# Kernel tuning notes

Hardware: AMD Instinct MI355X
Metric: run time of the kernel (lower is better)

## Reference

```python
import jax, jax.numpy as jnp
import numpy as np

EPS_COS = 1e-8   # torch F.cosine_similarity norm clamp
EPS_LN = 1e-5    # torch LayerNorm eps


def setup_inputs() -> dict:
    key = jax.random.key(0)
    ks = jax.random.split(key, 8)
    B, P, T, D, H = 512, 200000, 4, 64, 256
    return {
        "target_feat": jax.random.normal(ks[0], (B, D), jnp.float32),
        "source_protos": jax.random.normal(ks[1], (P, T, D), jnp.float32),
        "W1": jax.random.normal(ks[2], (3 * D, H), jnp.float32) * 0.05,
        "b1": jnp.zeros((H,), jnp.float32),
        "ln_g": jnp.ones((H,), jnp.float32),
        "ln_b": jnp.zeros((H,), jnp.float32),
        "W2": jax.random.normal(ks[3], (H, H), jnp.float32) * 0.05,
        "b2": jnp.zeros((H,), jnp.float32),
        "W3": jax.random.normal(ks[4], (H, D), jnp.float32) * 0.05,
        "b3": jnp.zeros((D,), jnp.float32),
        "top_k": 3,
    }


def _layernorm(x, g, b):
    mu = jnp.mean(x, axis=-1, keepdims=True)
    var = jnp.mean(jnp.square(x - mu), axis=-1, keepdims=True)
    return (x - mu) * jax.lax.rsqrt(var + EPS_LN) * g + b


def reference(target_feat, source_protos, W1, b1, ln_g, ln_b, W2, b2, W3, b3, top_k):
    # --- retrieve_similar_prototypes (batched over B queries) ---
    centers = jnp.mean(source_protos, axis=1)              # [P, D]
    tn = target_feat / jnp.maximum(
        jnp.linalg.norm(target_feat, axis=-1, keepdims=True), EPS_COS)
    cn = centers / jnp.maximum(
        jnp.linalg.norm(centers, axis=-1, keepdims=True), EPS_COS)
    sims = jnp.einsum("bd,pd->bp", tn, cn)                 # [B, P] cosine sims
    top_vals, top_idx = jax.lax.top_k(sims, top_k)         # [B, K]
    similar_protos = centers[top_idx]                      # [B, K, D] gather

    # --- interpolate_new_prototype ---
    weights = jax.nn.softmax(top_vals, axis=-1)            # [B, K]
    weighted = jnp.einsum("bkd,bk->bd", similar_protos, weights)
    concat = jnp.concatenate(
        [weighted, similar_protos[:, 0], target_feat], axis=-1)  # [B, 3D]

    h = jax.nn.relu(_layernorm(concat @ W1 + b1, ln_g, ln_b))
    h = jax.nn.relu(h @ W2 + b2)
    new_proto = h @ W3 + b3                                # [B, D]
    return new_proto
```

## Files before the change

kernel.cpp:

```cpp
#include <hip/hip_runtime.h>

#define PTOT 200000
#define NB 512
#define DD 64
#define PT 256
#define NBLK ((PTOT + PT - 1) / PT)
#define NCAND 8

typedef __attribute__((ext_vector_type(4))) float f32x4;
typedef __attribute__((ext_vector_type(8))) __bf16 bf16x8;

__device__ __forceinline__ ushort f2bf(float f){
  uint u = __float_as_uint(f);
  u += 0x7FFFu + ((u >> 16) & 1u);
  return (ushort)(u >> 16);
}

__device__ __forceinline__ uint mkkey(float v, int plocal){
  uint u = __float_as_uint(v);
  u = (u & 0xFFFFFE00u) | (uint)plocal;
  return u ^ (uint)(((int)u >> 31) | 0x80000000);
}

__device__ __forceinline__ void ins3(uint& k0, uint& k1, uint& k2, uint key){
  uint t0 = k0 > key ? k0 : key;
  uint m0 = k0 > key ? key : k0;
  uint t1 = k1 > m0 ? k1 : m0;
  uint m1 = k1 > m0 ? m0 : k1;
  k2 = k2 > m1 ? k2 : m1;
  k1 = t1; k0 = t0;
}

__global__ __launch_bounds__(64) void k0_tn(const float* __restrict__ tf,
                                            float* __restrict__ tnf,
                                            ushort* __restrict__ tnb){
  int b = blockIdx.x, d = threadIdx.x;
  float v = tf[b * DD + d];
  float ss = v * v;
  #pragma unroll
  for (int m = 1; m < 64; m <<= 1) ss += __shfl_xor(ss, m, 64);
  float rn = 1.0f / fmaxf(sqrtf(ss), 1e-8f);
  float t = v * rn;
  tnf[b * DD + d] = t;
  tnb[b * DD + d] = f2bf(t);
}

__global__ __launch_bounds__(256) void k1_scan(const float* __restrict__ sp,
                                               const ushort* __restrict__ tnb,
                                               uint* __restrict__ cand){
  __shared__ ushort cn[PT * 64];
  __shared__ uint kbuf[4][NB][3];
  const int tid = threadIdx.x;
  const int blk = blockIdx.x;
  const int pbase = blk * PT;
  const int plim = min(PT, PTOT - pbase);

  {
    const int s = tid & 15;
    const int pg = tid >> 4;
    for (int pass = 0; pass < 16; ++pass){
      int pl = pass * 16 + pg;
      f32x4 c = {0.f, 0.f, 0.f, 0.f};
      if (pl < plim){
        const float* base = sp + (size_t)(pbase + pl) * 256 + s * 4;
        f32x4 a0 = *(const f32x4*)(base);
        f32x4 a1 = *(const f32x4*)(base + 64);
        f32x4 a2 = *(const f32x4*)(base + 128);
        f32x4 a3 = *(const f32x4*)(base + 192);
        c = ((a0 + a1) + (a2 + a3)) * 0.25f;
      }
      float ss2 = c.x*c.x + c.y*c.y + c.z*c.z + c.w*c.w;
      ss2 += __shfl_xor(ss2, 1, 64);
      ss2 += __shfl_xor(ss2, 2, 64);
      ss2 += __shfl_xor(ss2, 4, 64);
      ss2 += __shfl_xor(ss2, 8, 64);
      float rn = 1.0f / fmaxf(sqrtf(ss2), 1e-8f);
      ushort4 h;
      h.x = f2bf(c.x * rn); h.y = f2bf(c.y * rn);
      h.z = f2bf(c.z * rn); h.w = f2bf(c.w * rn);
      int byteo = (pl * 128 + s * 8) ^ ((pl & 7) << 4);
      *(ushort4*)((char*)cn + byteo) = h;
    }
  }
  __syncthreads();

  const int wave = tid >> 6;
  const int lane = tid & 63;
  const int l15 = lane & 15;
  const int lg  = lane >> 4;
  const int wpb = wave * 64;

  bf16x8 afrag[4][2];
  #pragma unroll
  for (int ps = 0; ps < 4; ++ps){
    #pragma unroll
    for (int kh = 0; kh < 2; ++kh){
      int p = wpb + ps * 16 + l15;
      int byteo = (p * 128 + (kh * 32 + lg * 8) * 2) ^ ((p & 7) << 4);
      afrag[ps][kh] = *(const bf16x8*)((const char*)cn + byteo);
    }
  }

  const int lbase = lg * 4;
  for (int bt = 0; bt < 32; ++bt){
    const ushort* tp = tnb + (size_t)(bt * 16 + l15) * 64 + lg * 8;
    bf16x8 bf0 = *(const bf16x8*)(tp);
    bf16x8 bf1 = *(const bf16x8*)(tp + 32);
    f32x4 acc[4];
    #pragma unroll
    for (int ps = 0; ps < 4; ++ps){
      f32x4 z = {0.f, 0.f, 0.f, 0.f};
      acc[ps] = __builtin_amdgcn_mfma_f32_16x16x32_bf16(afrag[ps][0], bf0, z, 0, 0, 0);
      acc[ps] = __builtin_amdgcn_mfma_f32_16x16x32_bf16(afrag[ps][1], bf1, acc[ps], 0, 0, 0);
    }
    uint k0 = 0, k1 = 0, k2 = 0;
    #pragma unroll
    for (int ps = 0; ps < 4; ++ps){
      #pragma unroll
      for (int j = 0; j < 4; ++j){
        int plocal = wpb + ps * 16 + lbase + j;
        uint key = mkkey(acc[ps][j], plocal);
        key = (plocal < plim) ? key : 0u;
        ins3(k0, k1, k2, key);
      }
    }
    #pragma unroll
    for (int m = 16; m <= 32; m <<= 1){
      uint o0 = (uint)__shfl_xor((int)k0, m, 64);
      uint o1 = (uint)__shfl_xor((int)k1, m, 64);
      uint o2 = (uint)__shfl_xor((int)k2, m, 64);
      ins3(k0, k1, k2, o0);
      ins3(k0, k1, k2, o1);
      ins3(k0, k1, k2, o2);
    }
    if (lane < 16){
      int b = bt * 16 + l15;
      kbuf[wave][b][0] = k0;
      kbuf[wave][b][1] = k1;
      kbuf[wave][b][2] = k2;
    }
  }
  __syncthreads();
  for (int b = tid; b < NB; b += 256){
    uint k0 = 0, k1 = 0, k2 = 0;
    #pragma unroll
    for (int w = 0; w < 4; ++w){
      ins3(k0, k1, k2, kbuf[w][b][0]);
      ins3(k0, k1, k2, kbuf[w][b][1]);
      ins3(k0, k1, k2, kbuf[w][b][2]);
    }
    uint* dst = cand + ((size_t)b * NBLK + blk) * 3;
    dst[0] = k0; dst[1] = k1; dst[2] = k2;
  }
}

__global__ __launch_bounds__(256) void k2_rerank(const uint* __restrict__ cand,
    const float* __restrict__ sp, const float* __restrict__ tnf,
    const float* __restrict__ tf, float* __restrict__ concat){
  __shared__ uint pool[NBLK * 3];
  __shared__ uint redk[4];
  __shared__ int redp[4];
  __shared__ int topp[NCAND];
  __shared__ float cen[NCAND][DD];
  __shared__ float esim[NCAND];
  __shared__ float wts[3];
  __shared__ int sel[3];
  const int b = blockIdx.x;
  const int tid = threadIdx.x;
  const int NP = NBLK * 3;
  for (int j = tid; j < NP; j += 256) pool[j] = cand[(size_t)b * NP + j];
  __syncthreads();
  const int lane = tid & 63, wave = tid >> 6;
  for (int it = 0; it < NCAND; ++it){
    uint bk = 0; int bp = 0;
    for (int j = tid; j < NP; j += 256){
      uint k = pool[j];
      if (k > bk){ bk = k; bp = j; }
    }
    #pragma unroll
    for (int m = 1; m < 64; m <<= 1){
      uint ok = (uint)__shfl_xor((int)bk, m, 64);
      int  op = __shfl_xor(bp, m, 64);
      if (ok > bk){ bk = ok; bp = op; }
    }
    if (lane == 0){ redk[wave] = bk; redp[wave] = bp; }
    __syncthreads();
    if (tid == 0){
      uint bbk = 0; int bbp = 0;
      #pragma unroll
      for (int w = 0; w < 4; ++w){
        if (redk[w] > bbk){ bbk = redk[w]; bbp = redp[w]; }
      }
      topp[it] = (bbp / 3) * PT + (int)(bbk & 0x1FFu);
      pool[bbp] = 0u;
    }
    __syncthreads();
  }
  for (int c = wave; c < NCAND; c += 4){
    int p = topp[c];
    const float* base = sp + (size_t)p * 256 + lane;
    float x = 0.25f * (base[0] + base[64] + base[128] + base[192]);
    float ss = x * x;
    float dt = x * tnf[b * DD + lane];
    #pragma unroll
    for (int m = 1; m < 64; m <<= 1){
      ss += __shfl_xor(ss, m, 64);
      dt += __shfl_xor(dt, m, 64);
    }
    cen[c][lane] = x;
    if (lane == 0) esim[c] = dt / fmaxf(sqrtf(ss), 1e-8f);
  }
  __syncthreads();
  if (tid == 0){
    float v0 = -3.0e38f, v1 = v0, v2 = v0;
    int s0 = 0, s1 = 0, s2 = 0;
    for (int c = 0; c < NCAND; ++c){
      float v = esim[c];
      if (v > v0){ v2=v1; s2=s1; v1=v0; s1=s0; v0=v; s0=c; }
      else if (v > v1){ v2=v1; s2=s1; v1=v; s1=c; }
      else if (v > v2){ v2=v; s2=c; }
    }
    float e1 = expf(v1 - v0), e2 = expf(v2 - v0);
    float inv = 1.0f / (1.0f + e1 + e2);
    wts[0] = inv; wts[1] = e1 * inv; wts[2] = e2 * inv;
    sel[0] = s0; sel[1] = s1; sel[2] = s2;
  }
  __syncthreads();
  if (tid < DD){
    float w0 = wts[0], w1 = wts[1], w2 = wts[2];
    float c0 = cen[sel[0]][tid], c1 = cen[sel[1]][tid], c2 = cen[sel[2]][tid];
    float* row = concat + (size_t)b * 192;
    row[tid]       = w0 * c0 + w1 * c1 + w2 * c2;
    row[DD + tid]  = c0;
    row[128 + tid] = tf[b * DD + tid];
  }
}

__global__ __launch_bounds__(256) void k3_mlp(const float* __restrict__ concat,
    const float* __restrict__ W1, const float* __restrict__ b1,
    const float* __restrict__ lng, const float* __restrict__ lnb,
    const float* __restrict__ W2, const float* __restrict__ b2,
    const float* __restrict__ W3, const float* __restrict__ b3,
    float* __restrict__ out){
  __shared__ float cc[4][192];
  __shared__ float h1[4][256];
  __shared__ float h2[4][256];
  const int tid = threadIdx.x;
  const int rb = blockIdx.x * 4;
  for (int j = tid; j < 4 * 192; j += 256)
    cc[j / 192][j % 192] = concat[(size_t)rb * 192 + j];
  __syncthreads();
  {
    const int h = tid;
    float a0 = b1[h]; float a1 = a0, a2 = a0, a3 = a0;
    for (int k = 0; k < 192; ++k){
      float w = W1[k * 256 + h];
      a0 = fmaf(cc[0][k], w, a0);
      a1 = fmaf(cc[1][k], w, a1);
      a2 = fmaf(cc[2][k], w, a2);
      a3 = fmaf(cc[3][k], w, a3);
    }
    h1[0][h] = a0; h1[1][h] = a1; h1[2][h] = a2; h1[3][h] = a3;
  }
  __syncthreads();
  {
    const int lane = tid & 63, w = tid >> 6;
    float v[4]; float s = 0.f, q = 0.f;
    #pragma unroll
    for (int j = 0; j < 4; ++j){
      v[j] = h1[w][lane + 64 * j];
      s += v[j]; q += v[j] * v[j];
    }
    #pragma unroll
    for (int m = 1; m < 64; m <<= 1){
      s += __shfl_xor(s, m, 64);
      q += __shfl_xor(q, m, 64);
    }
    float mu = s * (1.0f / 256.0f);
    float var = q * (1.0f / 256.0f) - mu * mu;
    float rs = rsqrtf(var + 1e-5f);
    #pragma unroll
    for (int j = 0; j < 4; ++j){
      int hh = lane + 64 * j;
      float y = (v[j] - mu) * rs * lng[hh] + lnb[hh];
      h1[w][hh] = fmaxf(y, 0.0f);
    }
  }
  __syncthreads();
  {
    const int h = tid;
    float a0 = b2[h]; float a1 = a0, a2 = a0, a3 = a0;
    for (int k = 0; k < 256; ++k){
      float w = W2[k * 256 + h];
      a0 = fmaf(h1[0][k], w, a0);
      a1 = fmaf(h1[1][k], w, a1);
      a2 = fmaf(h1[2][k], w, a2);
      a3 = fmaf(h1[3][k], w, a3);
    }
    h2[0][h] = fmaxf(a0, 0.f); h2[1][h] = fmaxf(a1, 0.f);
    h2[2][h] = fmaxf(a2, 0.f); h2[3][h] = fmaxf(a3, 0.f);
  }
  __syncthreads();
  {
    const int d = tid & 63, q = tid >> 6;
    float a = b3[d];
    for (int k = 0; k < 256; ++k)
      a = fmaf(h2[q][k], W3[k * 64 + d], a);
    out[(size_t)(rb + q) * 64 + d] = a;
  }
}

extern "C" void kernel_launch(void* const* d_in, const int* in_sizes, int n_in,
                              void* d_out, int out_size, void* d_ws, size_t ws_size,
                              hipStream_t stream){
  const float* tf = (const float*)d_in[0];
  const float* sp = (const float*)d_in[1];
  const float* W1 = (const float*)d_in[2];
  const float* b1 = (const float*)d_in[3];
  const float* lng = (const float*)d_in[4];
  const float* lnb = (const float*)d_in[5];
  const float* W2 = (const float*)d_in[6];
  const float* b2 = (const float*)d_in[7];
  const float* W3 = (const float*)d_in[8];
  const float* b3 = (const float*)d_in[9];
  float* out = (float*)d_out;

  char* ws = (char*)d_ws;
  const size_t off_tnb = 0;
  const size_t off_tnf = 65536;
  const size_t off_cand = 65536 + 131072;
  const size_t off_cc = off_cand + (size_t)NB * NBLK * 3 * 4;
  const size_t need = off_cc + (size_t)NB * 192 * 4;
  if (ws_size < need) return;

  ushort* tnb = (ushort*)(ws + off_tnb);
  float* tnf = (float*)(ws + off_tnf);
  uint* cand = (uint*)(ws + off_cand);
  float* cc = (float*)(ws + off_cc);

  k0_tn<<<NB, 64, 0, stream>>>(tf, tnf, tnb);
  k1_scan<<<NBLK, 256, 0, stream>>>(sp, tnb, cand);
  k2_rerank<<<NB, 256, 0, stream>>>(cand, sp, tnf, tf, cc);
  k3_mlp<<<NB / 4, 256, 0, stream>>>(cc, W1, b1, lng, lnb, W2, b2, W3, b3, out);
}
```

Before: 135.1 us.

## Split center computation into separate kernel and restructure scan per-wave over queries

```diff
diff --git a/kernel.cpp b/kernel.cpp
--- a/kernel.cpp
+++ b/kernel.cpp
@@ -45,6 +45,109 @@
   tnb[b * DD + d] = f2bf(t);
 }
 
+__global__ __launch_bounds__(256) void k1a_centers(const float* __restrict__ sp,
+                                                   ushort* __restrict__ cn){
+  int gid = blockIdx.x * 256 + threadIdx.x;
+  int p = gid >> 4, s = gid & 15;
+  f32x4 c = {0.f, 0.f, 0.f, 0.f};
+  if (p < PTOT){
+    const float* base = sp + (size_t)p * 256 + s * 4;
+    f32x4 a0 = *(const f32x4*)(base);
+    f32x4 a1 = *(const f32x4*)(base + 64);
+    f32x4 a2 = *(const f32x4*)(base + 128);
+    f32x4 a3 = *(const f32x4*)(base + 192);
+    c = ((a0 + a1) + (a2 + a3)) * 0.25f;
+  }
+  float ss = c.x*c.x + c.y*c.y + c.z*c.z + c.w*c.w;
+  ss += __shfl_xor(ss, 1, 64);
+  ss += __shfl_xor(ss, 2, 64);
+  ss += __shfl_xor(ss, 4, 64);
+  ss += __shfl_xor(ss, 8, 64);
+  float rn = 1.0f / fmaxf(sqrtf(ss), 1e-8f);
+  ushort4 h;
+  h.x = f2bf(c.x * rn); h.y = f2bf(c.y * rn);
+  h.z = f2bf(c.z * rn); h.w = f2bf(c.w * rn);
+  *(ushort4*)(cn + (size_t)p * 64 + s * 4) = h;
+}
+
+__global__ __launch_bounds__(256) void k1b_scan(const ushort* __restrict__ cn,
+                                                const ushort* __restrict__ tnb,
+                                                uint* __restrict__ cand){
+  __shared__ __align__(16) ushort lds[PT * 64];
+  const int tid = threadIdx.x;
+  const int blk = blockIdx.x;
+  const int pbase = blk * PT;
+
+  {
+    const char* src = (const char*)(cn + (size_t)pbase * 64);
+    #pragma unroll
+    for (int k = 0; k < 8; ++k){
+      int off = (k * 256 + tid) * 16;
+      f32x4 v = *(const f32x4*)(src + off);
+      int dst = off ^ (((off >> 7) & 7) << 4);
+      *(f32x4*)((char*)lds + dst) = v;
+    }
+  }
+  __syncthreads();
+
+  const int wave = tid >> 6;
+  const int lane = tid & 63;
+  const int l15 = lane & 15;
+  const int lg  = lane >> 4;
+
+  uint ka[8], kb[8], kc[8];
+  #pragma unroll
+  for (int i = 0; i < 8; ++i){ ka[i] = 0; kb[i] = 0; kc[i] = 0; }
+
+  for (int ch = 0; ch < 4; ++ch){
+    bf16x8 afrag[4][2];
+    #pragma unroll
+    for (int ps = 0; ps < 4; ++ps){
+      int p = ch * 64 + ps * 16 + l15;
+      #pragma unroll
+      for (int kh = 0; kh < 2; ++kh){
+        int byteo = (p * 128 + (kh * 32 + lg * 8) * 2) ^ ((p & 7) << 4);
+        afrag[ps][kh] = *(const bf16x8*)((const char*)lds + byteo);
+      }
+    }
+    #pragma unroll
+    for (int bt8 = 0; bt8 < 8; ++bt8){
+      int bt = wave * 8 + bt8;
+      const ushort* tp = tnb + (size_t)(bt * 16 + l15) * 64 + lg * 8;
+      bf16x8 bf0 = *(const bf16x8*)(tp);
+      bf16x8 bf1 = *(const bf16x8*)(tp + 32);
+      #pragma unroll
+      for (int ps = 0; ps < 4; ++ps){
+        f32x4 z = {0.f, 0.f, 0.f, 0.f};
+        f32x4 acc = __builtin_amdgcn_mfma_f32_16x16x32_bf16(afrag[ps][0], bf0, z, 0, 0, 0);
+        acc = __builtin_amdgcn_mfma_f32_16x16x32_bf16(afrag[ps][1], bf1, acc, 0, 0, 0);
+        #pragma unroll
+        for (int j = 0; j < 4; ++j){
+          int plocal = ch * 64 + ps * 16 + lg * 4 + j;
+          uint key = (__float_as_uint(fmaxf(acc[j], 0.0f)) & 0xFFFFFE00u) | (uint)plocal;
+          ins3(ka[bt8], kb[bt8], kc[bt8], key);
+        }
+      }
+    }
+  }
+  #pragma unroll
+  for (int bt8 = 0; bt8 < 8; ++bt8){
+    uint a0 = ka[bt8], a1 = kb[bt8], a2 = kc[bt8];
+    #pragma unroll
+    for (int m = 16; m <= 32; m <<= 1){
+      uint o0 = (uint)__shfl_xor((int)a0, m, 64);
+      uint o1 = (uint)__shfl_xor((int)a1, m, 64);
+      uint o2 = (uint)__shfl_xor((int)a2, m, 64);
+      ins3(a0, a1, a2, o0); ins3(a0, a1, a2, o1); ins3(a0, a1, a2, o2);
+    }
+    if (lane < 16){
+      int b = (wave * 8 + bt8) * 16 + l15;
+      uint* dst = cand + ((size_t)b * NBLK + blk) * 3;
+      dst[0] = a0; dst[1] = a1; dst[2] = a2;
+    }
+  }
+}
+
 __global__ __launch_bounds__(256) void k1_scan(const float* __restrict__ sp,
                                                const ushort* __restrict__ tnb,
                                                uint* __restrict__ cand){
@@ -54,7 +157,6 @@
   const int blk = blockIdx.x;
   const int pbase = blk * PT;
   const int plim = min(PT, PTOT - pbase);
-
   {
     const int s = tid & 15;
     const int pg = tid >> 4;
@@ -83,13 +185,11 @@
     }
   }
   __syncthreads();
-
   const int wave = tid >> 6;
   const int lane = tid & 63;
   const int l15 = lane & 15;
   const int lg  = lane >> 4;
   const int wpb = wave * 64;
-
   bf16x8 afrag[4][2];
   #pragma unroll
   for (int ps = 0; ps < 4; ++ps){
@@ -100,7 +200,6 @@
       afrag[ps][kh] = *(const bf16x8*)((const char*)cn + byteo);
     }
   }
-
   const int lbase = lg * 4;
   for (int bt = 0; bt < 32; ++bt){
     const ushort* tp = tnb + (size_t)(bt * 16 + l15) * 64 + lg * 8;
@@ -191,7 +290,8 @@
       for (int w = 0; w < 4; ++w){
         if (redk[w] > bbk){ bbk = redk[w]; bbp = redp[w]; }
       }
-      topp[it] = (bbp / 3) * PT + (int)(bbk & 0x1FFu);
+      int p = (bbp / 3) * PT + (int)(bbk & 0x1FFu);
+      topp[it] = min(p, PTOT - 1);
       pool[bbp] = 0u;
     }
     __syncthreads();
@@ -326,20 +426,36 @@
   float* out = (float*)d_out;
 
   char* ws = (char*)d_ws;
-  const size_t off_tnb = 0;
-  const size_t off_tnf = 65536;
-  const size_t off_cand = 65536 + 131072;
-  const size_t off_cc = off_cand + (size_t)NB * NBLK * 3 * 4;
-  const size_t need = off_cc + (size_t)NB * 192 * 4;
-  if (ws_size < need) return;
+  const size_t off_tnb  = 0;
+  const size_t off_tnf  = 65536;
+  const size_t off_cn   = 65536 + 131072;
+  const size_t cn_bytes = (size_t)NBLK * PT * 64 * 2;
+  const size_t off_cand = off_cn + cn_bytes;
+  const size_t off_cc   = off_cand + (size_t)NB * NBLK * 3 * 4;
+  const size_t need_new = off_cc + (size_t)NB * 192 * 4;
+
+  const size_t f_off_cand = 65536 + 131072;
+  const size_t f_off_cc   = f_off_cand + (size_t)NB * NBLK * 3 * 4;
+  const size_t need_old   = f_off_cc + (size_t)NB * 192 * 4;
 
   ushort* tnb = (ushort*)(ws + off_tnb);
   float* tnf = (float*)(ws + off_tnf);
-  uint* cand = (uint*)(ws + off_cand);
-  float* cc = (float*)(ws + off_cc);
-
-  k0_tn<<<NB, 64, 0, stream>>>(tf, tnf, tnb);
-  k1_scan<<<NBLK, 256, 0, stream>>>(sp, tnb, cand);
-  k2_rerank<<<NB, 256, 0, stream>>>(cand, sp, tnf, tf, cc);
-  k3_mlp<<<NB / 4, 256, 0, stream>>>(cc, W1, b1, lng, lnb, W2, b2, W3, b3, out);
-}
+
+  if (ws_size >= need_new){
+    ushort* cnb = (ushort*)(ws + off_cn);
+    uint* cand = (uint*)(ws + off_cand);
+    float* cc = (float*)(ws + off_cc);
+    k0_tn<<<NB, 64, 0, stream>>>(tf, tnf, tnb);
+    k1a_centers<<<(NBLK * PT) / 16, 256, 0, stream>>>(sp, cnb);
+    k1b_scan<<<NBLK, 256, 0, stream>>>(cnb, tnb, cand);
+    k2_rerank<<<NB, 256, 0, stream>>>(cand, sp, tnf, tf, cc);
+    k3_mlp<<<NB / 4, 256, 0, stream>>>(cc, W1, b1, lng, lnb, W2, b2, W3, b3, out);
+  } else if (ws_size >= need_old){
+    uint* cand = (uint*)(ws + f_off_cand);
+    float* cc = (float*)(ws + f_off_cc);
+    k0_tn<<<NB, 64, 0, stream>>>(tf, tnf, tnb);
+    k1_scan<<<NBLK, 256, 0, stream>>>(sp, tnb, cand);
+    k2_rerank<<<NB, 256, 0, stream>>>(cand, sp, tnf, tf, cc);
+    k3_mlp<<<NB / 4, 256, 0, stream>>>(cc, W1, b1, lng, lnb, W2, b2, W3, b3, out);
+  }
+}
```

Measured after the change: 130.4 us. 1.04x faster.

## Split center normalization into streaming kernel, restructure scan, fuse rerank into MLP

Applied to the files above, without the earlier changes.

```diff
diff --git a/kernel.cpp b/kernel.cpp
--- a/kernel.cpp
+++ b/kernel.cpp
@@ -5,7 +5,9 @@
 #define DD 64
 #define PT 256
 #define NBLK ((PTOT + PT - 1) / PT)
+#define NPAD (NBLK * PT)
 #define NCAND 8
+#define NP3 (NBLK * 3)
 
 typedef __attribute__((ext_vector_type(4))) float f32x4;
 typedef __attribute__((ext_vector_type(8))) __bf16 bf16x8;
@@ -14,12 +16,6 @@
   uint u = __float_as_uint(f);
   u += 0x7FFFu + ((u >> 16) & 1u);
   return (ushort)(u >> 16);
-}
-
-__device__ __forceinline__ uint mkkey(float v, int plocal){
-  uint u = __float_as_uint(v);
-  u = (u & 0xFFFFFE00u) | (uint)plocal;
-  return u ^ (uint)(((int)u >> 31) | 0x80000000);
 }
 
 __device__ __forceinline__ void ins3(uint& k0, uint& k1, uint& k2, uint key){
@@ -31,55 +27,65 @@
   k1 = t1; k0 = t0;
 }
 
-__global__ __launch_bounds__(64) void k0_tn(const float* __restrict__ tf,
-                                            float* __restrict__ tnf,
-                                            ushort* __restrict__ tnb){
-  int b = blockIdx.x, d = threadIdx.x;
-  float v = tf[b * DD + d];
-  float ss = v * v;
-  #pragma unroll
-  for (int m = 1; m < 64; m <<= 1) ss += __shfl_xor(ss, m, 64);
-  float rn = 1.0f / fmaxf(sqrtf(ss), 1e-8f);
-  float t = v * rn;
-  tnf[b * DD + d] = t;
-  tnb[b * DD + d] = f2bf(t);
-}
-
-__global__ __launch_bounds__(256) void k1_scan(const float* __restrict__ sp,
-                                               const ushort* __restrict__ tnb,
-                                               uint* __restrict__ cand){
-  __shared__ ushort cn[PT * 64];
-  __shared__ uint kbuf[4][NB][3];
-  const int tid = threadIdx.x;
-  const int blk = blockIdx.x;
-  const int pbase = blk * PT;
-  const int plim = min(PT, PTOT - pbase);
-
-  {
-    const int s = tid & 15;
-    const int pg = tid >> 4;
-    for (int pass = 0; pass < 16; ++pass){
-      int pl = pass * 16 + pg;
-      f32x4 c = {0.f, 0.f, 0.f, 0.f};
-      if (pl < plim){
-        const float* base = sp + (size_t)(pbase + pl) * 256 + s * 4;
+__global__ __launch_bounds__(256) void kA_stream(const float* __restrict__ sp,
+                                                 const float* __restrict__ tf,
+                                                 ushort* __restrict__ cn,
+                                                 float* __restrict__ tnf,
+                                                 ushort* __restrict__ tnb){
+  const int tglob = blockIdx.x * 256 + threadIdx.x;
+  const int s = tglob & 15;
+  const int NG = NPAD + NB;
+  const int gstride = (2048 * 256) / 16;
+  for (int g = tglob >> 4; g < NG; g += gstride){
+    f32x4 c = {0.f, 0.f, 0.f, 0.f};
+    if (g < NPAD){
+      if (g < PTOT){
+        const float* base = sp + (size_t)g * 256 + s * 4;
         f32x4 a0 = *(const f32x4*)(base);
         f32x4 a1 = *(const f32x4*)(base + 64);
         f32x4 a2 = *(const f32x4*)(base + 128);
         f32x4 a3 = *(const f32x4*)(base + 192);
         c = ((a0 + a1) + (a2 + a3)) * 0.25f;
       }
-      float ss2 = c.x*c.x + c.y*c.y + c.z*c.z + c.w*c.w;
-      ss2 += __shfl_xor(ss2, 1, 64);
-      ss2 += __shfl_xor(ss2, 2, 64);
-      ss2 += __shfl_xor(ss2, 4, 64);
-      ss2 += __shfl_xor(ss2, 8, 64);
-      float rn = 1.0f / fmaxf(sqrtf(ss2), 1e-8f);
-      ushort4 h;
-      h.x = f2bf(c.x * rn); h.y = f2bf(c.y * rn);
-      h.z = f2bf(c.z * rn); h.w = f2bf(c.w * rn);
-      int byteo = (pl * 128 + s * 8) ^ ((pl & 7) << 4);
-      *(ushort4*)((char*)cn + byteo) = h;
+    } else {
+      c = *(const f32x4*)(tf + (g - NPAD) * 64 + s * 4);
+    }
+    float ss = c.x*c.x + c.y*c.y + c.z*c.z + c.w*c.w;
+    ss += __shfl_xor(ss, 1, 64);
+    ss += __shfl_xor(ss, 2, 64);
+    ss += __shfl_xor(ss, 4, 64);
+    ss += __shfl_xor(ss, 8, 64);
+    float rn = 1.0f / fmaxf(sqrtf(ss), 1e-8f);
+    float n0 = c.x * rn, n1 = c.y * rn, n2 = c.z * rn, n3 = c.w * rn;
+    ushort4 h;
+    h.x = f2bf(n0); h.y = f2bf(n1); h.z = f2bf(n2); h.w = f2bf(n3);
+    if (g < NPAD){
+      *(ushort4*)(cn + (size_t)g * 64 + s * 4) = h;
+    } else {
+      int b = g - NPAD;
+      f32x4 t = {n0, n1, n2, n3};
+      *(f32x4*)(tnf + b * 64 + s * 4) = t;
+      *(ushort4*)(tnb + b * 64 + s * 4) = h;
+    }
+  }
+}
+
+__global__ __launch_bounds__(256) void kB_scan(const ushort* __restrict__ cn,
+                                               const ushort* __restrict__ tnb,
+                                               uint* __restrict__ cand){
+  __shared__ __align__(16) ushort lds[PT * 64];
+  const int tid = threadIdx.x;
+  const int blk = blockIdx.x;
+  const int pbase = blk * PT;
+
+  {
+    const char* src = (const char*)(cn + (size_t)pbase * 64);
+    #pragma unroll
+    for (int k = 0; k < 8; ++k){
+      int off = (k * 256 + tid) * 16;
+      f32x4 v = *(const f32x4*)(src + off);
+      int dst = off ^ (((off >> 7) & 7) << 4);
+      *(f32x4*)((char*)lds + dst) = v;
     }
   }
   __syncthreads();
@@ -88,155 +94,63 @@
   const int lane = tid & 63;
   const int l15 = lane & 15;
   const int lg  = lane >> 4;
-  const int wpb = wave * 64;
-
-  bf16x8 afrag[4][2];
-  #pragma unroll
-  for (int ps = 0; ps < 4; ++ps){
-    #pragma unroll
-    for (int kh = 0; kh < 2; ++kh){
-      int p = wpb + ps * 16 + l15;
-      int byteo = (p * 128 + (kh * 32 + lg * 8) * 2) ^ ((p & 7) << 4);
-      afrag[ps][kh] = *(const bf16x8*)((const char*)cn + byteo);
-    }
-  }
-
-  const int lbase = lg * 4;
-  for (int bt = 0; bt < 32; ++bt){
-    const ushort* tp = tnb + (size_t)(bt * 16 + l15) * 64 + lg * 8;
-    bf16x8 bf0 = *(const bf16x8*)(tp);
-    bf16x8 bf1 = *(const bf16x8*)(tp + 32);
-    f32x4 acc[4];
+
+  uint ka[8], kb[8], kc[8];
+  #pragma unroll
+  for (int i = 0; i < 8; ++i){ ka[i] = 0; kb[i] = 0; kc[i] = 0; }
+
+  for (int ch = 0; ch < 4; ++ch){
+    bf16x8 afrag[4][2];
     #pragma unroll
     for (int ps = 0; ps < 4; ++ps){
-      f32x4 z = {0.f, 0.f, 0.f, 0.f};
-      acc[ps] = __builtin_amdgcn_mfma_f32_16x16x32_bf16(afrag[ps][0], bf0, z, 0, 0, 0);
-      acc[ps] = __builtin_amdgcn_mfma_f32_16x16x32_bf16(afrag[ps][1], bf1, acc[ps], 0, 0, 0);
-    }
-    uint k0 = 0, k1 = 0, k2 = 0;
-    #pragma unroll
-    for (int ps = 0; ps < 4; ++ps){
+      int p = ch * 64 + ps * 16 + l15;
       #pragma unroll
-      for (int j = 0; j < 4; ++j){
-        int plocal = wpb + ps * 16 + lbase + j;
-        uint key = mkkey(acc[ps][j], plocal);
-        key = (plocal < plim) ? key : 0u;
-        ins3(k0, k1, k2, key);
+      for (int kh = 0; kh < 2; ++kh){
+        int byteo = (p * 128 + (kh * 32 + lg * 8) * 2) ^ ((p & 7) << 4);
+        afrag[ps][kh] = *(const bf16x8*)((const char*)lds + byteo);
       }
     }
     #pragma unroll
+    for (int bt8 = 0; bt8 < 8; ++bt8){
+      int bt = wave * 8 + bt8;
+      const ushort* tp = tnb + (size_t)(bt * 16 + l15) * 64 + lg * 8;
+      bf16x8 bf0 = *(const bf16x8*)(tp);
+      bf16x8 bf1 = *(const bf16x8*)(tp + 32);
+      #pragma unroll
+      for (int ps = 0; ps < 4; ++ps){
+        f32x4 z = {0.f, 0.f, 0.f, 0.f};
+        f32x4 acc = __builtin_amdgcn_mfma_f32_16x16x32_bf16(afrag[ps][0], bf0, z, 0, 0, 0);
+        acc = __builtin_amdgcn_mfma_f32_16x16x32_bf16(afrag[ps][1], bf1, acc, 0, 0, 0);
+        #pragma unroll
+        for (int j = 0; j < 4; ++j){
+          int plocal = ch * 64 + ps * 16 + lg * 4 + j;
+          uint key = (__float_as_uint(fmaxf(acc[j], 0.0f)) & 0xFFFFFE00u) | (uint)plocal;
+          ins3(ka[bt8], kb[bt8], kc[bt8], key);
+        }
+      }
+    }
+  }
+  #pragma unroll
+  for (int bt8 = 0; bt8 < 8; ++bt8){
+    uint a0 = ka[bt8], a1 = kb[bt8], a2 = kc[bt8];
+    #pragma unroll
     for (int m = 16; m <= 32; m <<= 1){
-      uint o0 = (uint)__shfl_xor((int)k0, m, 64);
-      uint o1 = (uint)__shfl_xor((int)k1, m, 64);
-      uint o2 = (uint)__shfl_xor((int)k2, m, 64);
-      ins3(k0, k1, k2, o0);
-      ins3(k0, k1, k2, o1);
-      ins3(k0, k1, k2, o2);
+      uint o0 = (uint)__shfl_xor((int)a0, m, 64);
+      uint o1 = (uint)__shfl_xor((int)a1, m, 64);
+      uint o2 = (uint)__shfl_xor((int)a2, m, 64);
+      ins3(a0, a1, a2, o0); ins3(a0, a1, a2, o1); ins3(a0, a1, a2, o2);
     }
     if (lane < 16){
-      int b = bt * 16 + l15;
-      kbuf[wave][b][0] = k0;
-      kbuf[wave][b][1] = k1;
-      kbuf[wave][b][2] = k2;
-    }
-  }
-  __syncthreads();
-  for (int b = tid; b < NB; b += 256){
-    uint k0 = 0, k1 = 0, k2 = 0;
-    #pragma unroll
-    for (int w = 0; w < 4; ++w){
-      ins3(k0, k1, k2, kbuf[w][b][0]);
-      ins3(k0, k1, k2, kbuf[w][b][1]);
-      ins3(k0, k1, k2, kbuf[w][b][2]);
-    }
-    uint* dst = cand + ((size_t)b * NBLK + blk) * 3;
-    dst[0] = k0; dst[1] = k1; dst[2] = k2;
-  }
-}
-
-__global__ __launch_bounds__(256) void k2_rerank(const uint* __restrict__ cand,
+      int b = (wave * 8 + bt8) * 16 + l15;
+      uint* dst = cand + ((size_t)b * NBLK + blk) * 3;
+      dst[0] = a0; dst[1] = a1; dst[2] = a2;
+    }
+  }
+}
+
+__global__ __launch_bounds__(256) void kC_fuse(const uint* __restrict__ cand,
     const float* __restrict__ sp, const float* __restrict__ tnf,
-    const float* __restrict__ tf, float* __restrict__ concat){
-  __shared__ uint pool[NBLK * 3];
-  __shared__ uint redk[4];
-  __shared__ int redp[4];
-  __shared__ int topp[NCAND];
-  __shared__ float cen[NCAND][DD];
-  __shared__ float esim[NCAND];
-  __shared__ float wts[3];
-  __shared__ int sel[3];
-  const int b = blockIdx.x;
-  const int tid = threadIdx.x;
-  const int NP = NBLK * 3;
-  for (int j = tid; j < NP; j += 256) pool[j] = cand[(size_t)b * NP + j];
-  __syncthreads();
-  const int lane = tid & 63, wave = tid >> 6;
-  for (int it = 0; it < NCAND; ++it){
-    uint bk = 0; int bp = 0;
-    for (int j = tid; j < NP; j += 256){
-      uint k = pool[j];
-      if (k > bk){ bk = k; bp = j; }
-    }
-    #pragma unroll
-    for (int m = 1; m < 64; m <<= 1){
-      uint ok = (uint)__shfl_xor((int)bk, m, 64);
-      int  op = __shfl_xor(bp, m, 64);
-      if (ok > bk){ bk = ok; bp = op; }
-    }
-    if (lane == 0){ redk[wave] = bk; redp[wave] = bp; }
-    __syncthreads();
-    if (tid == 0){
-      uint bbk = 0; int bbp = 0;
-      #pragma unroll
-      for (int w = 0; w < 4; ++w){
-        if (redk[w] > bbk){ bbk = redk[w]; bbp = redp[w]; }
-      }
-      topp[it] = (bbp / 3) * PT + (int)(bbk & 0x1FFu);
-      pool[bbp] = 0u;
-    }
-    __syncthreads();
-  }
-  for (int c = wave; c < NCAND; c += 4){
-    int p = topp[c];
-    const float* base = sp + (size_t)p * 256 + lane;
-    float x = 0.25f * (base[0] + base[64] + base[128] + base[192]);
-    float ss = x * x;
-    float dt = x * tnf[b * DD + lane];
-    #pragma unroll
-    for (int m = 1; m < 64; m <<= 1){
-      ss += __shfl_xor(ss, m, 64);
-      dt += __shfl_xor(dt, m, 64);
-    }
-    cen[c][lane] = x;
-    if (lane == 0) esim[c] = dt / fmaxf(sqrtf(ss), 1e-8f);
-  }
-  __syncthreads();
-  if (tid == 0){
-    float v0 = -3.0e38f, v1 = v0, v2 = v0;
-    int s0 = 0, s1 = 0, s2 = 0;
-    for (int c = 0; c < NCAND; ++c){
-      float v = esim[c];
-      if (v > v0){ v2=v1; s2=s1; v1=v0; s1=s0; v0=v; s0=c; }
-      else if (v > v1){ v2=v1; s2=s1; v1=v; s1=c; }
-      else if (v > v2){ v2=v; s2=c; }
-    }
-    float e1 = expf(v1 - v0), e2 = expf(v2 - v0);
-    float inv = 1.0f / (1.0f + e1 + e2);
-    wts[0] = inv; wts[1] = e1 * inv; wts[2] = e2 * inv;
-    sel[0] = s0; sel[1] = s1; sel[2] = s2;
-  }
-  __syncthreads();
-  if (tid < DD){
-    float w0 = wts[0], w1 = wts[1], w2 = wts[2];
-    float c0 = cen[sel[0]][tid], c1 = cen[sel[1]][tid], c2 = cen[sel[2]][tid];
-    float* row = concat + (size_t)b * 192;
-    row[tid]       = w0 * c0 + w1 * c1 + w2 * c2;
-    row[DD + tid]  = c0;
-    row[128 + tid] = tf[b * DD + tid];
-  }
-}
-
-__global__ __launch_bounds__(256) void k3_mlp(const float* __restrict__ concat,
+    const float* __restrict__ tf,
     const float* __restrict__ W1, const float* __restrict__ b1,
     const float* __restrict__ lng, const float* __restrict__ lnb,
     const float* __restrict__ W2, const float* __restrict__ b2,
@@ -246,25 +160,87 @@
   __shared__ float h1[4][256];
   __shared__ float h2[4][256];
   const int tid = threadIdx.x;
+  const int lane = tid & 63;
+  const int w = tid >> 6;
   const int rb = blockIdx.x * 4;
-  for (int j = tid; j < 4 * 192; j += 256)
-    cc[j / 192][j % 192] = concat[(size_t)rb * 192 + j];
-  __syncthreads();
+  const int b = rb + w;
+
+  const uint* crow = cand + (size_t)b * NP3;
+  uint k0 = 0, k1 = 0, k2 = 0; int j0 = 0, j1 = 0, j2 = 0;
+  for (int i = 0; i < (NP3 + 63) / 64; ++i){
+    int j = lane + i * 64;
+    uint k = (j < NP3) ? crow[j] : 0u;
+    if (k > k0){ k2=k1; j2=j1; k1=k0; j1=j0; k0=k; j0=j; }
+    else if (k > k1){ k2=k1; j2=j1; k1=k; j1=j; }
+    else if (k > k2){ k2=k; j2=j; }
+  }
+  int pcand[NCAND];
+  #pragma unroll
+  for (int it = 0; it < NCAND; ++it){
+    uint wk = k0; int wj = j0;
+    #pragma unroll
+    for (int m = 1; m < 64; m <<= 1){
+      uint ok = (uint)__shfl_xor((int)wk, m, 64);
+      int  oj = __shfl_xor(wj, m, 64);
+      if (ok > wk || (ok == wk && oj > wj)){ wk = ok; wj = oj; }
+    }
+    pcand[it] = min((wj / 3) * PT + (int)(wk & 0x1FFu), PTOT - 1);
+    if (k0 == wk && j0 == wj){ k0=k1; j0=j1; k1=k2; j1=j2; k2=0; j2=0; }
+  }
+  float xc[NCAND], es[NCAND];
+  const float tno = tnf[b * 64 + lane];
+  #pragma unroll
+  for (int c = 0; c < NCAND; ++c){
+    const float* base = sp + (size_t)pcand[c] * 256 + lane;
+    float x = 0.25f * (base[0] + base[64] + base[128] + base[192]);
+    float ss = x * x;
+    float dt = x * tno;
+    #pragma unroll
+    for (int m = 1; m < 64; m <<= 1){
+      ss += __shfl_xor(ss, m, 64);
+      dt += __shfl_xor(dt, m, 64);
+    }
+    xc[c] = x;
+    es[c] = dt / fmaxf(sqrtf(ss), 1e-8f);
+  }
+  float v0 = -3.0e38f, v1 = v0, v2 = v0;
+  int s0 = 0, s1 = 0, s2 = 0;
+  #pragma unroll
+  for (int c = 0; c < NCAND; ++c){
+    float v = es[c];
+    if (v > v0){ v2=v1; s2=s1; v1=v0; s1=s0; v0=v; s0=c; }
+    else if (v > v1){ v2=v1; s2=s1; v1=v; s1=c; }
+    else if (v > v2){ v2=v; s2=c; }
+  }
+  float e1 = expf(v1 - v0), e2 = expf(v2 - v0);
+  float inv = 1.0f / (1.0f + e1 + e2);
+  float w0 = inv, w1 = e1 * inv, w2 = e2 * inv;
+  float wsum = 0.f, ctop = 0.f;
+  #pragma unroll
+  for (int c = 0; c < NCAND; ++c){
+    float coef = (c == s0) ? w0 : (c == s1) ? w1 : (c == s2) ? w2 : 0.f;
+    wsum = fmaf(xc[c], coef, wsum);
+    ctop += (c == s0) ? xc[c] : 0.f;
+  }
+  cc[w][lane]       = wsum;
+  cc[w][64 + lane]  = ctop;
+  cc[w][128 + lane] = tf[b * 64 + lane];
+  __syncthreads();
+
   {
     const int h = tid;
     float a0 = b1[h]; float a1 = a0, a2 = a0, a3 = a0;
     for (int k = 0; k < 192; ++k){
-      float w = W1[k * 256 + h];
-      a0 = fmaf(cc[0][k], w, a0);
-      a1 = fmaf(cc[1][k], w, a1);
-      a2 = fmaf(cc[2][k], w, a2);
-      a3 = fmaf(cc[3][k], w, a3);
+      float wv = W1[k * 256 + h];
+      a0 = fmaf(cc[0][k], wv, a0);
+      a1 = fmaf(cc[1][k], wv, a1);
+      a2 = fmaf(cc[2][k], wv, a2);
+      a3 = fmaf(cc[3][k], wv, a3);
     }
     h1[0][h] = a0; h1[1][h] = a1; h1[2][h] = a2; h1[3][h] = a3;
   }
   __syncthreads();
   {
-    const int lane = tid & 63, w = tid >> 6;
     float v[4]; float s = 0.f, q = 0.f;
     #pragma unroll
     for (int j = 0; j < 4; ++j){
@@ -291,11 +267,11 @@
     const int h = tid;
     float a0 = b2[h]; float a1 = a0, a2 = a0, a3 = a0;
     for (int k = 0; k < 256; ++k){
-      float w = W2[k * 256 + h];
-      a0 = fmaf(h1[0][k], w, a0);
-      a1 = fmaf(h1[1][k], w, a1);
-      a2 = fmaf(h1[2][k], w, a2);
-      a3 = fmaf(h1[3][k], w, a3);
+      float wv = W2[k * 256 + h];
+      a0 = fmaf(h1[0][k], wv, a0);
+      a1 = fmaf(h1[1][k], wv, a1);
+      a2 = fmaf(h1[2][k], wv, a2);
+      a3 = fmaf(h1[3][k], wv, a3);
     }
     h2[0][h] = fmaxf(a0, 0.f); h2[1][h] = fmaxf(a1, 0.f);
     h2[2][h] = fmaxf(a2, 0.f); h2[3][h] = fmaxf(a3, 0.f);
@@ -326,20 +302,21 @@
   float* out = (float*)d_out;
 
   char* ws = (char*)d_ws;
-  const size_t off_tnb = 0;
-  const size_t off_tnf = 65536;
-  const size_t off_cand = 65536 + 131072;
-  const size_t off_cc = off_cand + (size_t)NB * NBLK * 3 * 4;
-  const size_t need = off_cc + (size_t)NB * 192 * 4;
+  const size_t off_tnb  = 0;
+  const size_t off_tnf  = 65536;
+  const size_t off_cn   = 65536 + 131072;
+  const size_t cn_bytes = (size_t)NPAD * 64 * 2;
+  const size_t off_cand = off_cn + cn_bytes;
+  const size_t need = off_cand + (size_t)NB * NP3 * 4;
   if (ws_size < need) return;
 
   ushort* tnb = (ushort*)(ws + off_tnb);
-  float* tnf = (float*)(ws + off_tnf);
-  uint* cand = (uint*)(ws + off_cand);
-  float* cc = (float*)(ws + off_cc);
-
-  k0_tn<<<NB, 64, 0, stream>>>(tf, tnf, tnb);
-  k1_scan<<<NBLK, 256, 0, stream>>>(sp, tnb, cand);
-  k2_rerank<<<NB, 256, 0, stream>>>(cand, sp, tnf, tf, cc);
-  k3_mlp<<<NB / 4, 256, 0, stream>>>(cc, W1, b1, lng, lnb, W2, b2, W3, b3, out);
-}
+  float*  tnf = (float*)(ws + off_tnf);
+  ushort* cnb = (ushort*)(ws + off_cn);
+  uint*   cand = (uint*)(ws + off_cand);
+
+  kA_stream<<<2048, 256, 0, stream>>>(sp, tf, cnb, tnf, tnb);
+  kB_scan<<<NBLK, 256, 0, stream>>>(cnb, tnb, cand);
+  kC_fuse<<<NB / 4, 256, 0, stream>>>(cand, sp, tnf, tf,
+                                      W1, b1, lng, lnb, W2, b2, W3, b3, out);
+}
```

After: 131.3 us. 1.03x faster.
